# Kernel optimization log

Measured on AMD Instinct MI355X. Metric: run time of the kernel, lower is better.

Reference implementation:

```python
import jax, jax.numpy as jnp
import numpy as np

LSTM = 400   # lstm_size
M = 20       # output_mixture_components
K = 10       # attention_mixture_components
A = 73       # alphabet_size


def setup_inputs() -> dict:
    key = jax.random.key(0)
    ks = jax.random.split(key, 24)
    B, T, U = 128, 800, 64

    def p(k, shape, scale=0.05):
        return jax.random.normal(k, shape, dtype=jnp.float32) * scale

    in1 = 3 + A                 # lstm1 input: [window, x]
    in2 = 3 + LSTM + A          # lstm2 input: [x, h1, window]
    in3 = 3 + 2 * LSTM + A      # lstm3 input: [x, h1, h2, window]

    inp = {
        "inputs": jax.random.normal(ks[0], (B, T, 3), dtype=jnp.float32) * 0.1,
        "char_seq": jax.random.randint(ks[1], (B, U), 0, A),
        "char_seq_lengths": jax.random.randint(ks[2], (B,), U // 2, U + 1),
        "bias": jnp.full((B,), 0.5, dtype=jnp.float32),
        # LSTMCell params (torch layout: gates order i,f,g,o)
        "Wih1": p(ks[3], (4 * LSTM, in1)), "Whh1": p(ks[4], (4 * LSTM, LSTM)),
        "bih1": p(ks[5], (4 * LSTM,)),    "bhh1": p(ks[6], (4 * LSTM,)),
        "Wih2": p(ks[7], (4 * LSTM, in2)), "Whh2": p(ks[8], (4 * LSTM, LSTM)),
        "bih2": p(ks[9], (4 * LSTM,)),    "bhh2": p(ks[10], (4 * LSTM,)),
        "Wih3": p(ks[11], (4 * LSTM, in3)), "Whh3": p(ks[12], (4 * LSTM, LSTM)),
        "bih3": p(ks[13], (4 * LSTM,)),    "bhh3": p(ks[14], (4 * LSTM,)),
        # Attention: h1 -> (alpha_hat, beta_hat, kappa_hat), 3K outputs
        "Wa": p(ks[15], (3 * K, LSTM)), "ba": p(ks[16], (3 * K,)),
        # GMM head: [h1,h2,h3] -> 6M+1 params
        "Wg": p(ks[17], (6 * M + 1, 3 * LSTM)), "bg": p(ks[18], (6 * M + 1,)),
    }
    return inp


def _lstm_cell(x, h, c, Wih, Whh, bih, bhh):
    gates = x @ Wih.T + bih + h @ Whh.T + bhh
    i, f, g, o = jnp.split(gates, 4, axis=-1)
    c = jax.nn.sigmoid(f) * c + jax.nn.sigmoid(i) * jnp.tanh(g)
    h = jax.nn.sigmoid(o) * jnp.tanh(c)
    return h, c


def reference(inputs, char_seq, char_seq_lengths, bias,
              Wih1, Whh1, bih1, bhh1,
              Wih2, Whh2, bih2, bhh2,
              Wih3, Whh3, bih3, bhh3,
              Wa, ba, Wg, bg):
    B, T, _ = inputs.shape
    U = char_seq.shape[1]
    oh = jax.nn.one_hot(char_seq, A, dtype=jnp.float32)            # [B,U,A]
    u = jnp.arange(U, dtype=jnp.float32)                            # [U]
    umask = (u[None, :] < char_seq_lengths[:, None].astype(jnp.float32)).astype(jnp.float32)
    bias_c = bias[:, None]

    def step(carry, x_t):
        h1, c1, h2, c2, h3, c3, window, kappa = carry
        h1, c1 = _lstm_cell(jnp.concatenate([window, x_t], 1), h1, c1, Wih1, Whh1, bih1, bhh1)
        # Gaussian-mixture attention window (Graves 2013)
        ap = h1 @ Wa.T + ba                                         # [B,3K]
        alpha_h, beta_h, kappa_h = jnp.split(ap, 3, axis=1)
        alpha = jnp.exp(alpha_h)
        beta = jnp.exp(beta_h)
        kappa = kappa + jnp.exp(kappa_h)                            # [B,K]
        # phi[b,u] = sum_k alpha exp(-beta (kappa-u)^2)
        g = jnp.exp(-beta[:, :, None] * (kappa[:, :, None] - u) ** 2)  # [B,K,U]
        phi = jnp.einsum('bk,bku->bu', alpha, g) * umask
        window = jnp.einsum('bu,bua->ba', phi, oh)                  # [B,A]
        h2, c2 = _lstm_cell(jnp.concatenate([x_t, h1, window], 1), h2, c2, Wih2, Whh2, bih2, bhh2)
        h3, c3 = _lstm_cell(jnp.concatenate([x_t, h1, h2, window], 1), h3, c3, Wih3, Whh3, bih3, bhh3)
        # GMM output layer with sampling bias
        out = jnp.concatenate([h1, h2, h3], 1) @ Wg.T + bg          # [B,6M+1]
        pi_hat = out[:, :M]
        mus = out[:, M:3 * M]
        sig_hat = out[:, 3 * M:5 * M]
        rho_hat = out[:, 5 * M:6 * M]
        e_hat = out[:, 6 * M:]
        pis = jax.nn.softmax(pi_hat * (1.0 + bias_c), axis=-1)
        sigmas = jnp.exp(sig_hat - bias_c)
        rhos = jnp.tanh(rho_hat)
        es = jax.nn.sigmoid(e_hat)
        return (h1, c1, h2, c2, h3, c3, window, kappa), (pis, sigmas, rhos, mus, es)

    z = lambda d: jnp.zeros((B, d), dtype=jnp.float32)
    carry0 = (z(LSTM), z(LSTM), z(LSTM), z(LSTM), z(LSTM), z(LSTM), z(A), z(K))
    _, outs = jax.lax.scan(step, carry0, jnp.swapaxes(inputs, 0, 1))
    pis, sigmas, rhos, mus, es = (jnp.swapaxes(o, 0, 1) for o in outs)  # [B,T,*]
    return pis, sigmas, rhos, mus, es
```

## Files before the change

kernel.cpp:

```cpp
#include <hip/hip_runtime.h>
#include <stdint.h>

typedef short s8v __attribute__((ext_vector_type(8)));
typedef _Float16 h8v __attribute__((ext_vector_type(8)));
typedef float f4v __attribute__((ext_vector_type(4)));
typedef unsigned short u16;
typedef unsigned int u32;
typedef unsigned long long u64;

#define TT 800
#define BB 128
#define UU 64
#define ALP 73
#define DD 400

#define G_BATCH 32
#define N_CLUS 4
#define N_MEM 50
#define NTHREADS 256

#define CX0 0
#define CX1 32
#define CWIN 64
#define CWINLO 160
#define CH1 256
#define CH2 672
#define CH3 1088
#define ACT_STRIDE 3072

#define NC1 17
#define NC2 30
#define NC3 43
#define NCO 39
#define NCA 13
#define F1 5
#define F2 8
#define F3 11
#define FA 4
#define FO 10

#define ACT_BYTES (32*ACT_STRIDE)
#define H1LO_OFF ACT_BYTES
#define H1LO_STRIDE 896
#define RBUF_OFF (H1LO_OFF + 32*H1LO_STRIDE)
#define ABK_OFF (RBUF_OFF + 16384)
#define WINS_OFF (ABK_OFF + 3840)
#define CHAR_OFF (RBUF_OFF + 32768)
#define LENS_OFF (CHAR_OFF + 2048)
#define BIASC_OFF (LENS_OFF + 128)
#define BCI_OFF (BIASC_OFF + 128)
#define BAS_OFF (BCI_OFF + 384)
#define BGS_OFF (BAS_OFF + 128)
#define LDS_TOTAL (BGS_OFF + 128)

#define OFF_SIG ((size_t)BB*TT*20)
#define OFF_RHO ((size_t)BB*TT*60)
#define OFF_MU  ((size_t)BB*TT*80)
#define OFF_ES  ((size_t)BB*TT*120)

#define HBUF_U32 25600

#define MFMA16(A,B,C) __builtin_amdgcn_mfma_f32_16x16x32_f16(__builtin_bit_cast(h8v,(A)),__builtin_bit_cast(h8v,(B)),(C),0,0,0)

#define AST(p,v) __hip_atomic_store((p),(v),__ATOMIC_RELAXED,__HIP_MEMORY_SCOPE_AGENT)
#define ALD(p)   __hip_atomic_load((p),__ATOMIC_RELAXED,__HIP_MEMORY_SCOPE_AGENT)

__device__ __forceinline__ u16 f16b(float x) {
  _Float16 h = (_Float16)x;
  return __builtin_bit_cast(u16, h);
}
__device__ __forceinline__ float f2f(u16 h) {
  return (float)__builtin_bit_cast(_Float16, h);
}
__device__ __forceinline__ float sigm(float x) { return 1.f / (1.f + __expf(-x)); }
__device__ __forceinline__ float tanhe(float x) {
  float e = __expf(-2.f * fabsf(x));
  float r = (1.f - e) / (1.f + e);
  return (x < 0.f) ? -r : r;
}
__device__ __forceinline__ int imin(int a, int b) { return a < b ? a : b; }
__device__ __forceinline__ int lstm_row(int mem, int n, int r) {
  return (n*2 + (r>>3))*400 + mem*8 + (r&7);
}
__device__ __forceinline__ int out_orow(int rc) {
  if (rc < 20) return rc;
  if (rc < 60) return 60 + (rc-20);
  if (rc < 80) return 100 + (rc-60);
  if (rc < 120) return 20 + (rc-80);
  if (rc == 120) return 120;
  return -1;
}
__device__ __forceinline__ s8v gath(const float* W, int ld, int grow, int cb, int valid, int k0) {
  union { s8v v; u16 u[8]; } r;
  #pragma unroll
  for (int j = 0; j < 8; ++j) {
    int k = k0 + j;
    float x = 0.f;
    if (grow >= 0 && k < valid) x = W[(size_t)grow * ld + cb + k];
    r.u[j] = f16b(x);
  }
  return r.v;
}
__device__ __forceinline__ s8v gathlo(const float* W, int ld, int grow, int cb, int valid, int k0) {
  union { s8v v; u16 u[8]; } r;
  #pragma unroll
  for (int j = 0; j < 8; ++j) {
    int k = k0 + j;
    float x = 0.f;
    if (grow >= 0 && k < valid) x = W[(size_t)grow * ld + cb + k];
    u16 hi = f16b(x);
    r.u[j] = f16b(x - f2f(hi));
  }
  return r.v;
}

extern "C" __global__ __launch_bounds__(NTHREADS, 1)
void hwrnn(const float* __restrict__ xin, const int* __restrict__ chq,
           const int* __restrict__ lenq, const float* __restrict__ biasq,
           const float* __restrict__ Wih1, const float* __restrict__ Whh1,
           const float* __restrict__ bih1, const float* __restrict__ bhh1,
           const float* __restrict__ Wih2, const float* __restrict__ Whh2,
           const float* __restrict__ bih2, const float* __restrict__ bhh2,
           const float* __restrict__ Wih3, const float* __restrict__ Whh3,
           const float* __restrict__ bih3, const float* __restrict__ bhh3,
           const float* __restrict__ Wa, const float* __restrict__ ba,
           const float* __restrict__ Wg, const float* __restrict__ bg,
           float* __restrict__ dout, u32* __restrict__ barr,
           u32* __restrict__ h1ring, u32* __restrict__ h2g, u32* __restrict__ h3g,
           u32* __restrict__ h1glo)
{
  extern __shared__ __align__(16) char sm[];
  const int tid = threadIdx.x;
  const int wv = tid >> 6;
  const int ln = tid & 63;
  const int cl = blockIdx.x & 3;
  const int mem = blockIdx.x >> 2;
  const int B0 = cl * G_BATCH;

  const int arow = ln & 15;
  const int k0 = (ln >> 4) * 8;
  const int ahi = (ln >> 4) * 16;
  const int axor = (ln & 7) << 4;
  const int rb0 = arow * ACT_STRIDE;
  const int rb1 = (16 + arow) * ACT_STRIDE;
  const int hb0 = H1LO_OFF + arow * H1LO_STRIDE;
  const int hb1 = H1LO_OFF + (16 + arow) * H1LO_STRIDE;
  const f4v az = {0.f, 0.f, 0.f, 0.f};

  for (int i = tid; i * 16 < RBUF_OFF; i += NTHREADS) *(f4v*)(sm + i*16) = az;
  for (int i = tid; i < 32*UU; i += NTHREADS) {
    int b = i >> 6, u = i & 63;
    ((unsigned char*)(sm + CHAR_OFF))[i] = (unsigned char)chq[(B0 + b)*UU + u];
  }
  if (tid < 32) {
    ((int*)(sm + LENS_OFF))[tid] = lenq[B0 + tid];
    ((float*)(sm + BIASC_OFF))[tid] = biasq[B0 + tid];
    ((float*)(sm + BAS_OFF))[tid] = (tid < 30) ? ba[tid] : 0.f;
    float v = 0.f;
    if (mem == 0) { int orow = out_orow(tid); if (orow >= 0) v = bg[orow]; }
    else if (mem >= 1 && mem <= 6 && tid < 16) {
      int orow = out_orow((mem+1)*16 + tid); if (orow >= 0) v = bg[orow];
    }
    ((float*)(sm + BGS_OFF))[tid] = v;
  }
  if (tid < 96) {
    int l = tid >> 5, r = tid & 31;
    int grow = lstm_row(mem, r >> 4, r & 15);
    const float* bi = (l == 0) ? bih1 : (l == 1) ? bih2 : bih3;
    const float* bh = (l == 0) ? bhh1 : (l == 1) ? bhh2 : bhh3;
    ((float*)(sm + BCI_OFF))[l*32 + r] = bi[grow] + bh[grow];
  }

  s8v wf1[F1][2], wf2[F2][2], wf3[F3][2], wfa[FA][2], walo[FA][2], wfo[2][FO];
  #pragma unroll
  for (int i = 0; i < F1; ++i) {
    int c = wv + 4*i;
    #pragma unroll
    for (int n = 0; n < 2; ++n) {
      s8v v = {0,0,0,0,0,0,0,0};
      if (c < NC1) {
        int grow = lstm_row(mem, n, arow);
        if (c == 0)      v = gath(Wih1, 76, grow, 73, 3, k0);
        else if (c <= 3) v = gath(Wih1, 76, grow, (c-1)*32, imin(32, 73-(c-1)*32), k0);
        else             v = gath(Whh1, 400, grow, (c-4)*32, imin(32, 400-(c-4)*32), k0);
      }
      wf1[i][n] = v;
    }
  }
  #pragma unroll
  for (int i = 0; i < F2; ++i) {
    int c = wv + 4*i;
    #pragma unroll
    for (int n = 0; n < 2; ++n) {
      s8v v = {0,0,0,0,0,0,0,0};
      if (c < NC2) {
        int grow = lstm_row(mem, n, arow);
        if (c == 0)       v = gath(Wih2, 476, grow, 0, 3, k0);
        else if (c <= 13) v = gath(Wih2, 476, grow, 3+32*(c-1), imin(32, 400-32*(c-1)), k0);
        else if (c <= 16) v = gath(Wih2, 476, grow, 403+32*(c-14), imin(32, 73-32*(c-14)), k0);
        else              v = gath(Whh2, 400, grow, 32*(c-17), imin(32, 400-32*(c-17)), k0);
      }
      wf2[i][n] = v;
    }
  }
  #pragma unroll
  for (int i = 0; i < F3; ++i) {
    int c = wv + 4*i;
    #pragma unroll
    for (int n = 0; n < 2; ++n) {
      s8v v = {0,0,0,0,0,0,0,0};
      if (c < NC3) {
        int grow = lstm_row(mem, n, arow);
        if (c == 0)       v = gath(Wih3, 876, grow, 0, 3, k0);
        else if (c <= 13) v = gath(Wih3, 876, grow, 3+32*(c-1), imin(32, 400-32*(c-1)), k0);
        else if (c <= 26) v = gath(Wih3, 876, grow, 403+32*(c-14), imin(32, 400-32*(c-14)), k0);
        else if (c <= 29) v = gath(Wih3, 876, grow, 803+32*(c-27), imin(32, 73-32*(c-27)), k0);
        else              v = gath(Whh3, 400, grow, 32*(c-30), imin(32, 400-32*(c-30)), k0);
      }
      wf3[i][n] = v;
    }
  }
  #pragma unroll
  for (int i = 0; i < FA; ++i) {
    int c = wv + 4*i;
    #pragma unroll
    for (int n = 0; n < 2; ++n) {
      s8v v = {0,0,0,0,0,0,0,0}, vl = v;
      if (c < NCA) {
        int rr = n*16 + arow;
        int grow = (rr < 30) ? rr : -1;
        v  = gath  (Wa, 400, grow, 32*c, imin(32, 400-32*c), k0);
        vl = gathlo(Wa, 400, grow, 32*c, imin(32, 400-32*c), k0);
      }
      wfa[i][n] = v; walo[i][n] = vl;
    }
  }
  #pragma unroll
  for (int o = 0; o < 2; ++o) {
    #pragma unroll
    for (int i = 0; i < FO; ++i) {
      s8v v = {0,0,0,0,0,0,0,0};
      int c = wv + 4*i;
      bool have = (mem == 0) || (mem >= 1 && mem <= 6 && o == 0);
      if (have && c < NCO) {
        int ct = (mem == 0) ? o : (mem + 1);
        int grow = out_orow(ct*16 + arow);
        if (c <= 12)      v = gath(Wg, 1200, grow, 32*c, imin(32, 400-32*c), k0);
        else if (c <= 25) v = gath(Wg, 1200, grow, 400+32*(c-13), imin(32, 400-32*(c-13)), k0);
        else              v = gath(Wg, 1200, grow, 800+32*(c-26), imin(32, 400-32*(c-26)), k0);
      }
      wfo[o][i] = v;
    }
  }

  auto LDA0 = [&](int cb2) -> s8v { return *(const s8v*)(sm + rb0 + ((cb2 + ahi) ^ axor)); };
  auto LDA1 = [&](int cb2) -> s8v { return *(const s8v*)(sm + rb1 + ((cb2 + ahi) ^ axor)); };
  auto LDL0 = [&](int cb2) -> s8v { return *(const s8v*)(sm + hb0 + ((cb2 + ahi) ^ axor)); };
  auto LDL1 = [&](int cb2) -> s8v { return *(const s8v*)(sm + hb1 + ((cb2 + ahi) ^ axor)); };
  auto WPART = [&](int slot, f4v a) {
    *(f4v*)(sm + RBUF_OFF + (((slot*4 + wv)*256) + (ln & 15)*16 + (ln >> 4)*4)*4) = a;
  };
  auto RBF = [&](int slot, int w, int col, int row) -> float {
    return ((float*)(sm + RBUF_OFF))[(slot*4 + w)*256 + col*16 + row];
  };
  auto RLD = [&](const u32* ring, int half) -> s8v {
    union { s8v v; u64 q[2]; } r;
    r.q[0] = ALD((const u64*)ring + ((size_t)(B0 + arow + 16*half)*DD + k0 >> 2));
    r.q[1] = ALD((const u64*)ring + ((size_t)(B0 + arow + 16*half)*DD + k0 + 4 >> 2));
    return r.v;
  };
  const int ub = tid >> 3, uu = tid & 7;
  auto LUPD = [&](int sb, int l, float& c, u32* hg, u32* hlo) {
    int mt = ub >> 4, rw = ub & 15;
    const float* bci = (const float*)(sm + BCI_OFF);
    float vi = bci[l*32 + uu], vf = bci[l*32 + 8 + uu];
    float vg = bci[l*32 + 16 + uu], vo = bci[l*32 + 24 + uu];
    #pragma unroll
    for (int w = 0; w < 4; ++w) {
      vi += RBF(sb + mt, w, uu, rw);
      vf += RBF(sb + mt, w, 8 + uu, rw);
      vg += RBF(sb + 2 + mt, w, uu, rw);
      vo += RBF(sb + 2 + mt, w, 8 + uu, rw);
    }
    c = sigm(vf)*c + sigm(vi)*tanhe(vg);
    float h = sigm(vo)*tanhe(c);
    u16 hb = f16b(h);
    float hl = h - f2f(hb);
    float ho = __shfl_xor(h, 1, 64);
    float hlo_o = __shfl_xor(hl, 1, 64);
    if (!(uu & 1)) {
      size_t gi = ((size_t)(B0 + ub)*DD + mem*8 + uu) >> 1;
      AST(hg + gi, (u32)hb | ((u32)f16b(ho) << 16));
      if (hlo) AST(hlo + gi, (u32)f16b(hl) | ((u32)f16b(hlo_o) << 16));
    }
  };
  auto STAGEH = [&](const u32* hg, int cbase) {
    u64 va[7], vb[7];
    #pragma unroll
    for (int s = 0; s < 7; ++s) {
      int idx = tid + s*NTHREADS;
      if (idx < 1600) {
        int b = idx / 50, c16 = idx % 50;
        const u64* p = (const u64*)(hg + (((size_t)(B0 + b)*DD + c16*8) >> 1));
        va[s] = ALD(p); vb[s] = ALD(p + 1);
      }
    }
    #pragma unroll
    for (int s = 0; s < 7; ++s) {
      int idx = tid + s*NTHREADS;
      if (idx < 1600) {
        int b = idx / 50, c16 = idx % 50;
        int off = b*ACT_STRIDE + ((2*(cbase + c16*8)) ^ ((b & 7) << 4));
        *(u64*)(sm + off) = va[s];
        *(u64*)(sm + off + 8) = vb[s];
      }
    }
  };
  auto STAGEHLO = [&](const u32* hg) {
    u64 va[7], vb[7];
    #pragma unroll
    for (int s = 0; s < 7; ++s) {
      int idx = tid + s*NTHREADS;
      if (idx < 1600) {
        int b = idx / 50, c16 = idx % 50;
        const u64* p = (const u64*)(hg + (((size_t)(B0 + b)*DD + c16*8) >> 1));
        va[s] = ALD(p); vb[s] = ALD(p + 1);
      }
    }
    #pragma unroll
    for (int s = 0; s < 7; ++s) {
      int idx = tid + s*NTHREADS;
      if (idx < 1600) {
        int b = idx / 50, c16 = idx % 50;
        int off = H1LO_OFF + b*H1LO_STRIDE + ((16*c16) ^ ((b & 7) << 4));
        *(u64*)(sm + off) = va[s];
        *(u64*)(sm + off + 8) = vb[s];
      }
    }
  };
  u32* cA = barr + cl*64;
  auto ARRIVE = [&](u32* ctr) {
    asm volatile("s_waitcnt vmcnt(0)" ::: "memory");
    __syncthreads();
    if (tid == 0) __hip_atomic_fetch_add(ctr, 1u, __ATOMIC_RELAXED, __HIP_MEMORY_SCOPE_AGENT);
  };
  auto WAITC = [&](u32* ctr, u32 tgt) {
    if (tid == 0) {
      while (ALD(ctr) < tgt) __builtin_amdgcn_s_sleep(1);
    }
    __syncthreads();
  };

  __syncthreads();
  if (tid < 96) {
    int b = tid/3, cc = tid%3;
    float x = xin[((size_t)(B0+b)*TT)*3 + cc];
    int off = b*ACT_STRIDE + ((2*(CX0 + cc)) ^ ((b&7)<<4));
    *(u16*)(sm + off) = f16b(x);
  }
  __syncthreads();

  float c1 = 0.f, c2 = 0.f, c3 = 0.f, kap0 = 0.f, kap1 = 0.f;

  for (int t = 0; t <= TT + 1; ++t) {
    const int pc = t & 1, pp = pc ^ 1;
    const int xc = pc ? CX1 : CX0;
    const int xp = pp ? CX1 : CX0;
    u32* ring_w = h1ring + (size_t)(t & 3) * HBUF_U32;
    const u32* ring_o = h1ring + (size_t)((t + 2) & 3) * HBUF_U32;

    if (t < TT) {
      f4v a1[4] = {az, az, az, az};
      #pragma unroll
      for (int i = 0; i < F1; ++i) {
        int c = wv + 4*i;
        if (c < NC1) {
          int cb = (c == 0) ? xc : (c <= 3) ? (CWIN + 32*(c-1)) : (CH1 + 32*(c-4));
          int cb2 = 2*cb;
          s8v x0 = LDA0(cb2), x1 = LDA1(cb2);
          a1[0] = MFMA16(x0, wf1[i][0], a1[0]);
          a1[1] = MFMA16(x1, wf1[i][0], a1[1]);
          a1[2] = MFMA16(x0, wf1[i][1], a1[2]);
          a1[3] = MFMA16(x1, wf1[i][1], a1[3]);
          if (c >= 1) {
            s8v l0, l1;
            if (c <= 3) { int lb2 = 2*(CWINLO + 32*(c-1)); l0 = LDA0(lb2); l1 = LDA1(lb2); }
            else        { int lb2 = 64*(c-4);              l0 = LDL0(lb2); l1 = LDL1(lb2); }
            a1[0] = MFMA16(l0, wf1[i][0], a1[0]);
            a1[1] = MFMA16(l1, wf1[i][0], a1[1]);
            a1[2] = MFMA16(l0, wf1[i][1], a1[2]);
            a1[3] = MFMA16(l1, wf1[i][1], a1[3]);
          }
        }
      }
      WPART(0, a1[0]); WPART(1, a1[1]); WPART(2, a1[2]); WPART(3, a1[3]);
    }
    __syncthreads();
    if (t < TT) LUPD(0, 0, c1, ring_w, h1glo + (size_t)pc * HBUF_U32);
    ARRIVE(cA);

    WAITC(cA, (u32)(t + 1) * N_MEM);

    if (t >= 2) STAGEH(h3g + (size_t)pc * HBUF_U32, CH3);
    __syncthreads();

    if (t >= 2 && mem <= 6) {
      f4v ao[4] = {az, az, az, az};
      #pragma unroll
      for (int i = 0; i < FO; ++i) {
        int c = wv + 4*i;
        if (c < NCO) {
          s8v x0, x1;
          if (c <= 12) {
            const u32* rp = ring_o + (size_t)c * 16;
            x0 = RLD(rp, 0); x1 = RLD(rp, 1);
          } else {
            int cb = (c <= 25) ? (CH2 + 32*(c-13)) : (CH3 + 32*(c-26));
            x0 = LDA0(2*cb); x1 = LDA1(2*cb);
          }
          ao[0] = MFMA16(x0, wfo[0][i], ao[0]);
          ao[1] = MFMA16(x1, wfo[0][i], ao[1]);
          if (mem == 0) {
            ao[2] = MFMA16(x0, wfo[1][i], ao[2]);
            ao[3] = MFMA16(x1, wfo[1][i], ao[3]);
          }
        }
      }
      WPART(4, ao[0]); WPART(5, ao[1]);
      if (mem == 0) { WPART(6, ao[2]); WPART(7, ao[3]); }
    }
    __syncthreads();

    if (t >= 1 && t <= TT) STAGEH(h2g + (size_t)pp * HBUF_U32, CH2);
    if (t >= 2 && mem <= 6) {
      const float* bgs = (const float*)(sm + BGS_OFF);
      const float* bcv = (const float*)(sm + BIASC_OFF);
      int tt = t - 2;
      auto OSUM = [&](int rl, int b) -> float {
        int slot = 4 + ((mem == 0) ? ((rl >> 4)*2) : 0) + (b >> 4);
        float s = bgs[rl];
        #pragma unroll
        for (int w = 0; w < 4; ++w) s += RBF(slot, w, rl & 15, b & 15);
        return s;
      };
      if (mem == 0) {
        if (tid < 32) {
          int b = tid;
          float sc = 1.f + bcv[b];
          float pv[20]; float mx = -3e38f;
          #pragma unroll
          for (int r = 0; r < 20; ++r) { pv[r] = OSUM(r, b) * sc; mx = fmaxf(mx, pv[r]); }
          float den = 0.f;
          #pragma unroll
          for (int r = 0; r < 20; ++r) { pv[r] = __expf(pv[r] - mx); den += pv[r]; }
          float inv = 1.f / den;
          size_t ob = ((size_t)(B0 + b)*TT + tt);
          #pragma unroll
          for (int r = 0; r < 20; ++r) dout[ob*20 + r] = pv[r] * inv;
        }
        for (int idx = tid; idx < 12*32; idx += NTHREADS) {
          int rl = 20 + (idx >> 5), b = idx & 31;
          float v = OSUM(rl, b);
          size_t ob = ((size_t)(B0 + b)*TT + tt);
          dout[OFF_SIG + ob*40 + (rl - 20)] = __expf(v - bcv[b]);
        }
      } else {
        int RB = (mem + 1) * 16;
        for (int idx = tid; idx < 512; idx += NTHREADS) {
          int rl = idx >> 5, b = idx & 31;
          int rc = RB + rl;
          float v = OSUM(rl, b);
          size_t ob = ((size_t)(B0 + b)*TT + tt);
          if (rc < 60)        dout[OFF_SIG + ob*40 + (rc - 20)] = __expf(v - bcv[b]);
          else if (rc < 80)   dout[OFF_RHO + ob*20 + (rc - 60)] = tanhe(v);
          else if (rc < 120)  dout[OFF_MU  + ob*40 + (rc - 80)] = v;
          else if (rc == 120) dout[OFF_ES + ob] = sigm(v);
        }
      }
    }
    __syncthreads();

    f4v a2[4] = {az, az, az, az};
    if (t >= 1 && t <= TT) {
      f4v a3[4] = {az, az, az, az};
      #pragma unroll
      for (int i = 0; i < F3; ++i) {
        int c = wv + 4*i;
        if (c < NC3) {
          int cb = (c == 0) ? xp
                 : (c <= 13) ? (CH1 + 32*(c-1))
                 : (c <= 26) ? (CH2 + 32*(c-14))
                 : (c <= 29) ? (CWIN + 32*(c-27))
                 : (CH3 + 32*(c-30));
          int cb2 = 2*cb;
          s8v x0 = LDA0(cb2), x1 = LDA1(cb2);
          a3[0] = MFMA16(x0, wf3[i][0], a3[0]);
          a3[1] = MFMA16(x1, wf3[i][0], a3[1]);
          a3[2] = MFMA16(x0, wf3[i][1], a3[2]);
          a3[3] = MFMA16(x1, wf3[i][1], a3[3]);
          if ((c >= 1 && c <= 13) || (c >= 27 && c <= 29)) {
            s8v l0, l1;
            if (c <= 13) { int lb2 = 64*(c-1);               l0 = LDL0(lb2); l1 = LDL1(lb2); }
            else         { int lb2 = 2*(CWINLO + 32*(c-27)); l0 = LDA0(lb2); l1 = LDA1(lb2); }
            a3[0] = MFMA16(l0, wf3[i][0], a3[0]);
            a3[1] = MFMA16(l1, wf3[i][0], a3[1]);
            a3[2] = MFMA16(l0, wf3[i][1], a3[2]);
            a3[3] = MFMA16(l1, wf3[i][1], a3[3]);
          }
        }
      }
      WPART(4, a3[0]); WPART(5, a3[1]); WPART(6, a3[2]); WPART(7, a3[3]);
    }
    if (t < TT) {
      #pragma unroll
      for (int i = 0; i < F2; ++i) {
        int c = wv + 4*i;
        if (c < NC2 && (c == 0 || c >= 17)) {
          int cb = (c == 0) ? xc : (CH2 + 32*(c-17));
          int cb2 = 2*cb;
          s8v x0 = LDA0(cb2), x1 = LDA1(cb2);
          a2[0] = MFMA16(x0, wf2[i][0], a2[0]);
          a2[1] = MFMA16(x1, wf2[i][0], a2[1]);
          a2[2] = MFMA16(x0, wf2[i][1], a2[2]);
          a2[3] = MFMA16(x1, wf2[i][1], a2[3]);
        }
      }
    }
    __syncthreads();

    if (t < TT) { STAGEH(ring_w, CH1); STAGEHLO(h1glo + (size_t)pc * HBUF_U32); }
    if (t + 1 < TT && tid < 96) {
      int b = tid/3, cc = tid%3;
      float x = xin[((size_t)(B0+b)*TT + (t+1))*3 + cc];
      int off = b*ACT_STRIDE + ((2*(xp + cc)) ^ ((b&7)<<4));
      *(u16*)(sm + off) = f16b(x);
    }
    __syncthreads();

    if (t < TT) {
      f4v aa[4] = {az, az, az, az};
      #pragma unroll
      for (int i = 0; i < FA; ++i) {
        int c = wv + 4*i;
        if (c < NCA) {
          int cb2 = 2*(CH1 + 32*c);
          int lb2 = 64*c;
          s8v x0 = LDA0(cb2), x1 = LDA1(cb2);
          s8v l0 = LDL0(lb2), l1 = LDL1(lb2);
          aa[0] = MFMA16(x0, wfa[i][0], aa[0]);
          aa[1] = MFMA16(x1, wfa[i][0], aa[1]);
          aa[2] = MFMA16(x0, wfa[i][1], aa[2]);
          aa[3] = MFMA16(x1, wfa[i][1], aa[3]);
          aa[0] = MFMA16(l0, wfa[i][0], aa[0]);
          aa[1] = MFMA16(l1, wfa[i][0], aa[1]);
          aa[2] = MFMA16(l0, wfa[i][1], aa[2]);
          aa[3] = MFMA16(l1, wfa[i][1], aa[3]);
          aa[0] = MFMA16(x0, walo[i][0], aa[0]);
          aa[1] = MFMA16(x1, walo[i][0], aa[1]);
          aa[2] = MFMA16(x0, walo[i][1], aa[2]);
          aa[3] = MFMA16(x1, walo[i][1], aa[3]);
        }
      }
      WPART(0, aa[0]); WPART(1, aa[1]); WPART(2, aa[2]); WPART(3, aa[3]);
    }
    if (t >= 1 && t <= TT) LUPD(4, 2, c3, h3g + (size_t)pp * HBUF_U32, nullptr);
    __syncthreads();

    if (t < TT) {
      float* wins = (float*)(sm + WINS_OFF);
      for (int i = tid; i < 32*80; i += NTHREADS) wins[i] = 0.f;
      float* abk = (float*)(sm + ABK_OFF);
      const float* bas = (const float*)(sm + BAS_OFF);
      #pragma unroll
      for (int half = 0; half < 2; ++half) {
        int idx = tid + half*NTHREADS;
        if (idx < 320) {
          int b = idx & 31, j = idx >> 5;
          float ah = bas[j], bh = bas[10+j], kh = bas[20+j];
          #pragma unroll
          for (int w = 0; w < 4; ++w) {
            ah += RBF(0 + (b>>4), w, j, b & 15);
            if (j < 6) bh += RBF(0 + (b>>4), w, 10 + j, b & 15);
            else       bh += RBF(2 + (b>>4), w, j - 6, b & 15);
            kh += RBF(2 + (b>>4), w, 4 + j, b & 15);
          }
          float& kp = half ? kap1 : kap0;
          kp += __expf(kh);
          abk[0*320 + b*10 + j] = __expf(ah);
          abk[1*320 + b*10 + j] = __expf(bh);
          abk[2*320 + b*10 + j] = kp;
        }
      }
      __syncthreads();

      const unsigned char* chs = (const unsigned char*)(sm + CHAR_OFF);
      const int* lns = (const int*)(sm + LENS_OFF);
      for (int idx = tid; idx < 32*64; idx += NTHREADS) {
        int b = idx >> 6, u = idx & 63;
        if (u < lns[b]) {
          float ph = 0.f, fu = (float)u;
          #pragma unroll
          for (int j = 0; j < 10; ++j) {
            float d = abk[2*320 + b*10 + j] - fu;
            ph += abk[0*320 + b*10 + j] * __expf(-abk[1*320 + b*10 + j]*d*d);
          }
          atomicAdd(&wins[b*80 + (int)chs[b*64 + u]], ph);
        }
      }
      __syncthreads();

      for (int idx = tid; idx < 32*96; idx += NTHREADS) {
        int b = idx / 96, cc = idx % 96;
        float v = (cc < ALP) ? wins[b*80 + cc] : 0.f;
        u16 hi = f16b(v);
        u16 lo = f16b(v - f2f(hi));
        int sw = (b&7) << 4;
        *(u16*)(sm + b*ACT_STRIDE + ((2*(CWIN + cc)) ^ sw)) = hi;
        *(u16*)(sm + b*ACT_STRIDE + ((2*(CWINLO + cc)) ^ sw)) = lo;
      }
      __syncthreads();

      #pragma unroll
      for (int i = 0; i < F2; ++i) {
        int c = wv + 4*i;
        if (c >= 1 && c <= 16) {
          int cb = (c <= 13) ? (CH1 + 32*(c-1)) : (CWIN + 32*(c-14));
          int cb2 = 2*cb;
          s8v x0 = LDA0(cb2), x1 = LDA1(cb2);
          a2[0] = MFMA16(x0, wf2[i][0], a2[0]);
          a2[1] = MFMA16(x1, wf2[i][0], a2[1]);
          a2[2] = MFMA16(x0, wf2[i][1], a2[2]);
          a2[3] = MFMA16(x1, wf2[i][1], a2[3]);
          s8v l0, l1;
          if (c <= 13) { int lb2 = 64*(c-1);               l0 = LDL0(lb2); l1 = LDL1(lb2); }
          else         { int lb2 = 2*(CWINLO + 32*(c-14)); l0 = LDA0(lb2); l1 = LDA1(lb2); }
          a2[0] = MFMA16(l0, wf2[i][0], a2[0]);
          a2[1] = MFMA16(l1, wf2[i][0], a2[1]);
          a2[2] = MFMA16(l0, wf2[i][1], a2[2]);
          a2[3] = MFMA16(l1, wf2[i][1], a2[3]);
        }
      }
      WPART(0, a2[0]); WPART(1, a2[1]); WPART(2, a2[2]); WPART(3, a2[3]);
      __syncthreads();

      LUPD(0, 1, c2, h2g + (size_t)pc * HBUF_U32, nullptr);
    }
  }
}

extern "C" void kernel_launch(void* const* d_in, const int* in_sizes, int n_in,
                              void* d_out, int out_size, void* d_ws, size_t ws_size,
                              hipStream_t stream) {
  (void)in_sizes; (void)n_in; (void)out_size; (void)ws_size;
  const float* xin  = (const float*)d_in[0];
  const int*   chq  = (const int*)d_in[1];
  const int*   lnq  = (const int*)d_in[2];
  const float* bq   = (const float*)d_in[3];
  const float* Wih1 = (const float*)d_in[4];
  const float* Whh1 = (const float*)d_in[5];
  const float* bih1 = (const float*)d_in[6];
  const float* bhh1 = (const float*)d_in[7];
  const float* Wih2 = (const float*)d_in[8];
  const float* Whh2 = (const float*)d_in[9];
  const float* bih2 = (const float*)d_in[10];
  const float* bhh2 = (const float*)d_in[11];
  const float* Wih3 = (const float*)d_in[12];
  const float* Whh3 = (const float*)d_in[13];
  const float* bih3 = (const float*)d_in[14];
  const float* bhh3 = (const float*)d_in[15];
  const float* Wa   = (const float*)d_in[16];
  const float* ba   = (const float*)d_in[17];
  const float* Wg   = (const float*)d_in[18];
  const float* bg   = (const float*)d_in[19];
  float* dout = (float*)d_out;
  char* ws = (char*)d_ws;
  u32* barr   = (u32*)ws;
  u32* h1ring = (u32*)(ws + 4096);
  u32* h2g    = (u32*)(ws + 4096 + 409600);
  u32* h3g    = (u32*)(ws + 4096 + 409600 + 204800);
  u32* h1glo  = (u32*)(ws + 4096 + 409600 + 409600);

  hipMemsetAsync(ws, 0, 4096, stream);
  hipFuncSetAttribute(reinterpret_cast<const void*>(hwrnn),
                      hipFuncAttributeMaxDynamicSharedMemorySize, LDS_TOTAL);
  hipLaunchKernelGGL(hwrnn, dim3(N_CLUS * N_MEM), dim3(NTHREADS), LDS_TOTAL, stream,
                     xin, chq, lnq, bq, Wih1, Whh1, bih1, bhh1, Wih2, Whh2, bih2, bhh2,
                     Wih3, Whh3, bih3, bhh3, Wa, ba, Wg, bg, dout, barr,
                     h1ring, h2g, h3g, h1glo);
}
```

Before: 17.72 ms.

## Delay GMM output stage one step and move it before the cluster barrier wait

The GMM output projection now runs one timestep later (t-3), reading h1, h2 and h3 directly from deeper global ring buffers (8-deep for h1, 4-deep for h2/h3) instead of LDS-staged copies. This lets it execute before the cross-block barrier wait, hiding barrier latency behind output work. In exchange the workspace grows, the loop gains an extra iteration, and the output GEMM reads operands from global/L2 instead of LDS.

```diff
diff --git a/kernel.cpp b/kernel.cpp
--- a/kernel.cpp
+++ b/kernel.cpp
@@ -362,12 +362,11 @@
 
   float c1 = 0.f, c2 = 0.f, c3 = 0.f, kap0 = 0.f, kap1 = 0.f;
 
-  for (int t = 0; t <= TT + 1; ++t) {
+  for (int t = 0; t <= TT + 2; ++t) {
     const int pc = t & 1, pp = pc ^ 1;
     const int xc = pc ? CX1 : CX0;
     const int xp = pp ? CX1 : CX0;
-    u32* ring_w = h1ring + (size_t)(t & 3) * HBUF_U32;
-    const u32* ring_o = h1ring + (size_t)((t + 2) & 3) * HBUF_U32;
+    u32* ring_w = h1ring + (size_t)(t & 7) * HBUF_U32;
 
     if (t < TT) {
       f4v a1[4] = {az, az, az, az};
@@ -399,25 +398,19 @@
     if (t < TT) LUPD(0, 0, c1, ring_w, h1glo + (size_t)pc * HBUF_U32);
     ARRIVE(cA);
 
-    WAITC(cA, (u32)(t + 1) * N_MEM);
-
-    if (t >= 2) STAGEH(h3g + (size_t)pc * HBUF_U32, CH3);
-    __syncthreads();
-
-    if (t >= 2 && mem <= 6) {
+    if (t >= 3 && mem <= 6) {
+      const u32* r1 = h1ring + (size_t)((t + 5) & 7) * HBUF_U32;
+      const u32* r2 = h2g   + (size_t)((t + 1) & 3) * HBUF_U32;
+      const u32* r3 = h3g   + (size_t)((t + 1) & 3) * HBUF_U32;
       f4v ao[4] = {az, az, az, az};
       #pragma unroll
       for (int i = 0; i < FO; ++i) {
         int c = wv + 4*i;
         if (c < NCO) {
-          s8v x0, x1;
-          if (c <= 12) {
-            const u32* rp = ring_o + (size_t)c * 16;
-            x0 = RLD(rp, 0); x1 = RLD(rp, 1);
-          } else {
-            int cb = (c <= 25) ? (CH2 + 32*(c-13)) : (CH3 + 32*(c-26));
-            x0 = LDA0(2*cb); x1 = LDA1(2*cb);
-          }
+          const u32* rp = (c <= 12) ? (r1 + (size_t)c * 16)
+                        : (c <= 25) ? (r2 + (size_t)(c - 13) * 16)
+                        :             (r3 + (size_t)(c - 26) * 16);
+          s8v x0 = RLD(rp, 0), x1 = RLD(rp, 1);
           ao[0] = MFMA16(x0, wfo[0][i], ao[0]);
           ao[1] = MFMA16(x1, wfo[0][i], ao[1]);
           if (mem == 0) {
@@ -428,14 +421,10 @@
       }
       WPART(4, ao[0]); WPART(5, ao[1]);
       if (mem == 0) { WPART(6, ao[2]); WPART(7, ao[3]); }
-    }
-    __syncthreads();
-
-    if (t >= 1 && t <= TT) STAGEH(h2g + (size_t)pp * HBUF_U32, CH2);
-    if (t >= 2 && mem <= 6) {
+      __syncthreads();
       const float* bgs = (const float*)(sm + BGS_OFF);
       const float* bcv = (const float*)(sm + BIASC_OFF);
-      int tt = t - 2;
+      int tt = t - 3;
       auto OSUM = [&](int rl, int b) -> float {
         int slot = 4 + ((mem == 0) ? ((rl >> 4)*2) : 0) + (b >> 4);
         float s = bgs[rl];
@@ -478,6 +467,11 @@
         }
       }
     }
+
+    WAITC(cA, (u32)(t + 1) * N_MEM);
+
+    if (t >= 2 && t <= TT) STAGEH(h3g + (size_t)((t + 2) & 3) * HBUF_U32, CH3);
+    if (t >= 1 && t <= TT) STAGEH(h2g + (size_t)((t + 3) & 3) * HBUF_U32, CH2);
     __syncthreads();
 
     f4v a2[4] = {az, az, az, az};
@@ -563,7 +557,7 @@
       }
       WPART(0, aa[0]); WPART(1, aa[1]); WPART(2, aa[2]); WPART(3, aa[3]);
     }
-    if (t >= 1 && t <= TT) LUPD(4, 2, c3, h3g + (size_t)pp * HBUF_U32, nullptr);
+    if (t >= 1 && t <= TT) LUPD(4, 2, c3, h3g + (size_t)((t + 3) & 3) * HBUF_U32, nullptr);
     __syncthreads();
 
     if (t < TT) {
@@ -643,7 +637,7 @@
       WPART(0, a2[0]); WPART(1, a2[1]); WPART(2, a2[2]); WPART(3, a2[3]);
       __syncthreads();
 
-      LUPD(0, 1, c2, h2g + (size_t)pc * HBUF_U32, nullptr);
+      LUPD(0, 1, c2, h2g + (size_t)(t & 3) * HBUF_U32, nullptr);
     }
   }
 }
@@ -676,9 +670,9 @@
   char* ws = (char*)d_ws;
   u32* barr   = (u32*)ws;
   u32* h1ring = (u32*)(ws + 4096);
-  u32* h2g    = (u32*)(ws + 4096 + 409600);
-  u32* h3g    = (u32*)(ws + 4096 + 409600 + 204800);
-  u32* h1glo  = (u32*)(ws + 4096 + 409600 + 409600);
+  u32* h2g    = (u32*)(ws + 4096 + 819200);
+  u32* h3g    = (u32*)(ws + 4096 + 1232896 - 4096);
+  u32* h1glo  = (u32*)(ws + 1642496);
 
   hipMemsetAsync(ws, 0, 4096, stream);
   hipFuncSetAttribute(reinterpret_cast<const void*>(hwrnn),
```

Result: no change. 17.96 ms (+1.4%).
